# Performance work log

Hardware: AMD Instinct MI355X
Metric: run time of the kernel (lower is better)

## Reference

```python
import jax, jax.numpy as jnp
import numpy as np

DIM = 1024
DEPTH = 2
D_STATE = 16
EXPAND = 2            # standard Mamba expand factor -> d_inner = 2*dim
D_CONV = 4
DT_RANK = DIM // 16   # ceil(dim/16) = 64
D_INNER = DIM * EXPAND
BATCH = 2
SEQ = 1024


def setup_inputs() -> dict:
    key = jax.random.key(0)
    ks = jax.random.split(key, 8)
    def n(k, shape, scale):
        return jax.random.normal(k, shape, jnp.float32) * scale
    # A_log initialized as log(1..N) per channel (S4D-real init, as in mamba_ssm)
    A_log = jnp.tile(jnp.log(jnp.arange(1, D_STATE + 1, dtype=jnp.float32))[None, None, :],
                     (DEPTH, D_INNER, 1))
    return {
        "x": n(ks[0], (BATCH, SEQ, DIM), 1.0),
        "in_proj_w": n(ks[1], (DEPTH, 2 * D_INNER, DIM), DIM ** -0.5),
        "conv_w": n(ks[2], (DEPTH, D_INNER, D_CONV), D_CONV ** -0.5),
        "conv_b": jnp.zeros((DEPTH, D_INNER), jnp.float32),
        "x_proj_w": n(ks[3], (DEPTH, DT_RANK + 2 * D_STATE, D_INNER), D_INNER ** -0.5),
        "dt_proj_w": n(ks[4], (DEPTH, D_INNER, DT_RANK), DT_RANK ** -0.5),
        "dt_proj_b": n(ks[5], (DEPTH, D_INNER), 0.1),
        "A_log": A_log,
        "D": jnp.ones((DEPTH, D_INNER), jnp.float32),
        "out_proj_w": n(ks[6], (DEPTH, DIM, D_INNER), D_INNER ** -0.5),
    }


def _mamba_layer(x, in_w, cw, cb, xp_w, dtw, dtb, A_log, Dp, ow):
    # x: [B, L, dim]
    Bsz = x.shape[0]
    xz = jnp.einsum('bld,ed->ble', x, in_w)            # [B, L, 2*d_inner]
    xi, z = jnp.split(xz, 2, axis=-1)
    # causal depthwise conv1d over time
    xc = jnp.transpose(xi, (0, 2, 1))                  # [B, d_inner, L]
    xc = jax.lax.conv_general_dilated(xc, cw[:, None, :], (1,), [(D_CONV - 1, 0)],
                                      feature_group_count=D_INNER)
    xc = xc + cb[None, :, None]
    xc = jax.nn.silu(jnp.transpose(xc, (0, 2, 1)))     # [B, L, d_inner]
    # input-dependent dt, B, C
    x_dbl = jnp.einsum('bld,ed->ble', xc, xp_w)        # [B, L, dt_rank+2*N]
    dt_raw = x_dbl[..., :DT_RANK]
    Bm = x_dbl[..., DT_RANK:DT_RANK + D_STATE]         # [B, L, N]
    Cm = x_dbl[..., DT_RANK + D_STATE:]                # [B, L, N]
    dt = jax.nn.softplus(jnp.einsum('blr,dr->bld', dt_raw, dtw) + dtb)  # [B, L, d_inner]
    A = -jnp.exp(A_log)                                # [d_inner, N]
    dA = jnp.exp(dt[..., None] * A[None, None])        # [B, L, d_inner, N]
    dBu = dt[..., None] * Bm[:, :, None, :] * xc[..., None]

    def step(h, inp):
        dA_t, dBu_t, C_t = inp
        h = dA_t * h + dBu_t                           # [B, d_inner, N]
        y = jnp.einsum('bdn,bn->bd', h, C_t)
        return h, y

    h0 = jnp.zeros((Bsz, D_INNER, D_STATE), x.dtype)
    _, ys = jax.lax.scan(step, h0,
                         (dA.transpose(1, 0, 2, 3), dBu.transpose(1, 0, 2, 3),
                          Cm.transpose(1, 0, 2)))
    y = ys.transpose(1, 0, 2) + Dp[None, None, :] * xc
    y = y * jax.nn.silu(z)
    return jnp.einsum('bld,od->blo', y, ow)


def reference(x, in_proj_w, conv_w, conv_b, x_proj_w, dt_proj_w, dt_proj_b, A_log, D, out_proj_w):
    for i in range(DEPTH):
        x = _mamba_layer(x, in_proj_w[i], conv_w[i], conv_b[i], x_proj_w[i],
                         dt_proj_w[i], dt_proj_b[i], A_log[i], D[i], out_proj_w[i])
    return x
```

## Files before the change

kernel.cpp:

```cpp
#include <hip/hip_runtime.h>
#include <hip/hip_bf16.h>

typedef __hip_bfloat16 bf16;
typedef __attribute__((ext_vector_type(8))) short short8;
typedef __attribute__((ext_vector_type(4))) short shortx4;
typedef __attribute__((ext_vector_type(4))) float floatx4;

#define BATCH   2
#define SEQ     1024
#define DIM     1024
#define D_INNER 2048
#define D_STATE 16
#define DT_RANK 64
#define MROWS   (BATCH * SEQ)
#define CHUNK   32
#define NCHUNK  (SEQ / CHUNK)

__device__ __forceinline__ float bf2f(bf16 x) { return __bfloat162float(x); }
__device__ __forceinline__ bf16  f2bf(float x) { return __float2bfloat16(x); }
__device__ __forceinline__ short bfbits(float x) {
    bf16 b = __float2bfloat16(x); short s; __builtin_memcpy(&s, &b, 2); return s;
}
__device__ __forceinline__ float bits2f(short s) {
    bf16 b; __builtin_memcpy(&b, &s, 2); return __bfloat162float(b);
}

__device__ __forceinline__ void ld_lds16(const void* g, void* l) {
    __builtin_amdgcn_global_load_lds(
        (const __attribute__((address_space(1))) void*)g,
        (__attribute__((address_space(3))) void*)l, 16, 0, 0);
}

__device__ __forceinline__ void cast4(const float* in, short* o, int i) {
    floatx4 v = ((const floatx4*)in)[i];
    shortx4 r;
    r.x = bfbits(v.x); r.y = bfbits(v.y); r.z = bfbits(v.z); r.w = bfbits(v.w);
    ((shortx4*)o)[i] = r;
}
__global__ __launch_bounds__(256) void cast3_k(
    const float* __restrict__ a, short* __restrict__ oa, int na4,
    const float* __restrict__ b, short* __restrict__ ob, int nb4,
    const float* __restrict__ c, short* __restrict__ oc, int nc4)
{
    int i = blockIdx.x * 256 + threadIdx.x;
    if (i < na4) cast4(a, oa, i);
    else if (i - na4 < nb4) cast4(b, ob, i - na4);
    else if (i - na4 - nb4 < nc4) cast4(c, oc, i - na4 - nb4);
}

__device__ __forceinline__ short8 ld8_any(const void* p, size_t eoff, int is_f32) {
    if (is_f32) {
        const float* f = (const float*)p + eoff;
        floatx4 a = *(const floatx4*)f;
        floatx4 b = *(const floatx4*)(f + 4);
        short8 r;
        r[0] = bfbits(a[0]); r[1] = bfbits(a[1]); r[2] = bfbits(a[2]); r[3] = bfbits(a[3]);
        r[4] = bfbits(b[0]); r[5] = bfbits(b[1]); r[6] = bfbits(b[2]); r[7] = bfbits(b[3]);
        return r;
    } else {
        return *(const short8*)((const bf16*)p + eoff);
    }
}

__global__ __launch_bounds__(256) void gemm128(
    const bf16* __restrict__ A, int lda,
    const bf16* __restrict__ B, int ldb,
    float* __restrict__ Cf, bf16* __restrict__ Cb, int ldc,
    int kchunk, size_t psize)
{
    __shared__ short As[4][128 * 32];
    __shared__ short Bs[4][128 * 32];
    const int tid  = threadIdx.x;
    const int wave = tid >> 6;
    const int lane = tid & 63;
    const int m0 = blockIdx.y * 128;
    const int n0 = blockIdx.x * 128;
    const int wm = (wave & 1) * 64;
    const int wn = (wave >> 1) * 64;
    const int r16  = lane & 15;
    const int quad = lane >> 4;
    const int r0   = tid >> 2;
    const int csw   = (((tid & 3) ^ ((r0 >> 1) & 3)) << 3);
    const int swoff = ((quad ^ ((r16 >> 1) & 3)) << 3);
    const int kbeg = blockIdx.z * kchunk;
    const int nk   = kchunk >> 5;

    floatx4 acc[4][4] = {};

    auto STAGE = [&](int buf, int kk) {
        ld_lds16(A + (size_t)(m0 + r0) * lda + kk + csw,      &As[buf][tid * 8]);
        ld_lds16(A + (size_t)(m0 + r0 + 64) * lda + kk + csw, &As[buf][(tid + 256) * 8]);
        ld_lds16(B + (size_t)(n0 + r0) * ldb + kk + csw,      &Bs[buf][tid * 8]);
        ld_lds16(B + (size_t)(n0 + r0 + 64) * ldb + kk + csw, &Bs[buf][(tid + 256) * 8]);
    };
    auto COMPUTE = [&](int buf) {
        const short* Ab = As[buf];
        const short* Bb = Bs[buf];
        short8 af[4], bg[4];
#pragma unroll
        for (int i = 0; i < 4; i++) {
            af[i] = *(const short8*)(Ab + (wm + i * 16 + r16) * 32 + swoff);
            bg[i] = *(const short8*)(Bb + (wn + i * 16 + r16) * 32 + swoff);
        }
        __builtin_amdgcn_s_setprio(1);
#pragma unroll
        for (int i = 0; i < 4; i++)
#pragma unroll
            for (int j = 0; j < 4; j++)
                acc[i][j] = __builtin_amdgcn_mfma_f32_16x16x32_bf16(af[i], bg[j], acc[i][j], 0, 0, 0);
        __builtin_amdgcn_s_setprio(0);
    };

    STAGE(0, kbeg);
    STAGE(1, kbeg + 32);
    int it = 0;
    for (; it < nk - 2; ++it) {
        STAGE((it + 2) & 3, kbeg + (it + 2) * 32);
        asm volatile("s_waitcnt vmcnt(8) lgkmcnt(0)" ::: "memory");
        __builtin_amdgcn_s_barrier();
        __builtin_amdgcn_sched_barrier(0);
        COMPUTE(it & 3);
    }
    asm volatile("s_waitcnt vmcnt(4) lgkmcnt(0)" ::: "memory");
    __builtin_amdgcn_s_barrier();
    __builtin_amdgcn_sched_barrier(0);
    COMPUTE(it & 3);
    ++it;
    asm volatile("s_waitcnt vmcnt(0) lgkmcnt(0)" ::: "memory");
    __builtin_amdgcn_s_barrier();
    __builtin_amdgcn_sched_barrier(0);
    COMPUTE(it & 3);

    float* Cfp = Cf ? Cf + (size_t)blockIdx.z * psize : nullptr;
#pragma unroll
    for (int i = 0; i < 4; i++)
#pragma unroll
        for (int j = 0; j < 4; j++) {
            int gm = m0 + wm + i * 16 + quad * 4;
            int gn = n0 + wn + j * 16 + r16;
#pragma unroll
            for (int r = 0; r < 4; r++) {
                size_t o = (size_t)(gm + r) * ldc + gn;
                float v = acc[i][j][r];
                if (Cfp) Cfp[o] = v;
                if (Cb) Cb[o] = f2bf(v);
            }
        }
}

__global__ __launch_bounds__(256) void gemm_bt(
    const void* __restrict__ A, int a_f32, int lda,
    const void* __restrict__ B, int b_f32, int ldb,
    float* __restrict__ Cf, bf16* __restrict__ Cb, int ldc,
    int N, int K, size_t psize,
    const float* __restrict__ bias, int act)
{
    __shared__ short As[2][64][40];
    __shared__ short Bs[2][64][40];
    const int m0   = blockIdx.y * 64;
    const int n0   = blockIdx.x * 64;
    const int tid  = threadIdx.x;
    const int wave = tid >> 6;
    const int lane = tid & 63;
    const int srow = tid >> 2;
    const int scol = (tid & 3) << 3;
    const int r16  = lane & 15;
    const int quad = lane >> 4;
    const int kbeg = blockIdx.z * K;
    const int nst  = K >> 5;
    const int gn_b = n0 + srow;
    const bool bok = (gn_b < N);

    floatx4 acc[4] = {};

    short8 av = ld8_any(A, (size_t)(m0 + srow) * lda + kbeg + scol, a_f32);
    short8 bv = {};
    if (bok) bv = ld8_any(B, (size_t)gn_b * ldb + kbeg + scol, b_f32);

    for (int s = 0; s < nst; ++s) {
        const int cur = s & 1;
        *(short8*)(&As[cur][srow][scol]) = av;
        *(short8*)(&Bs[cur][srow][scol]) = bv;
        __syncthreads();
        if (s + 1 < nst) {
            int k1 = kbeg + (s + 1) * 32;
            av = ld8_any(A, (size_t)(m0 + srow) * lda + k1 + scol, a_f32);
            if (bok) bv = ld8_any(B, (size_t)gn_b * ldb + k1 + scol, b_f32);
        }
        short8 af = *(const short8*)(&As[cur][wave * 16 + r16][quad * 8]);
#pragma unroll
        for (int nt = 0; nt < 4; nt++) {
            short8 bq = *(const short8*)(&Bs[cur][nt * 16 + r16][quad * 8]);
            acc[nt] = __builtin_amdgcn_mfma_f32_16x16x32_bf16(af, bq, acc[nt], 0, 0, 0);
        }
    }

    float* Cfp = Cf ? Cf + (size_t)blockIdx.z * psize : nullptr;
#pragma unroll
    for (int nt = 0; nt < 4; nt++) {
        int gn = n0 + nt * 16 + r16;
        if (gn >= N) continue;
        float bsv = bias ? bias[gn] : 0.f;
#pragma unroll
        for (int r = 0; r < 4; r++) {
            int gm = m0 + wave * 16 + quad * 4 + r;
            float v = acc[nt][r] + bsv;
            if (act == 1) v = (v > 20.f) ? v : log1pf(__expf(v));
            size_t o = (size_t)gm * ldc + gn;
            if (Cfp) Cfp[o] = v;
            if (Cb) Cb[o] = f2bf(v);
        }
    }
}

__global__ __launch_bounds__(256) void reduceN_k(
    const float* __restrict__ part, size_t psize, int n, int np,
    float* __restrict__ of, bf16* __restrict__ ob)
{
    int i = blockIdx.x * 256 + threadIdx.x;
    if (i >= n) return;
    float v = 0.f;
    for (int j = 0; j < np; j++) v += part[i + (size_t)j * psize];
    if (of) of[i] = v;
    if (ob) ob[i] = f2bf(v);
}

__global__ __launch_bounds__(256) void conv_silu_k(
    const bf16* __restrict__ xz, const float* __restrict__ cw,
    const float* __restrict__ cb, bf16* __restrict__ xcb)
{
    int idx = blockIdx.x * 256 + threadIdx.x;
    int d   = (idx & 255) << 3;
    int bt  = idx >> 8;
    int t   = bt & (SEQ - 1);

    float s[8];
    floatx4 cb0 = *(const floatx4*)(cb + d);
    floatx4 cb1 = *(const floatx4*)(cb + d + 4);
#pragma unroll
    for (int i = 0; i < 4; i++) { s[i] = cb0[i]; s[i + 4] = cb1[i]; }

    floatx4 w[8];
#pragma unroll
    for (int i = 0; i < 8; i++) w[i] = *(const floatx4*)(cw + (d + i) * 4);

#pragma unroll
    for (int j = 0; j < 4; j++) {
        int tt = t - 3 + j;
        if (tt >= 0) {
            short8 v = *(const short8*)&xz[(size_t)(bt - 3 + j) * 4096 + d];
#pragma unroll
            for (int i = 0; i < 8; i++) s[i] += w[i][j] * bits2f(v[i]);
        }
    }
    short8 r;
#pragma unroll
    for (int i = 0; i < 8; i++) {
        float sig = 1.f / (1.f + __expf(-s[i]));
        r[i] = bfbits(s[i] * sig);
    }
    *(short8*)&xcb[(size_t)bt * D_INNER + d] = r;
}

__global__ __launch_bounds__(256) void scan1_k(
    const float* __restrict__ dtf, const bf16* __restrict__ xcb,
    const float* __restrict__ xdbl, const float* __restrict__ Alog,
    float* __restrict__ chunk_sdt, float* __restrict__ chunk_S)
{
    __shared__ float dt_s[CHUNK][256];
    __shared__ short xc_s[CHUNK][256];
    __shared__ float B_s[CHUNK][16];
    const int tid = threadIdx.x;
    const int d0  = blockIdx.x * 256;
    const int d   = d0 + tid;
    const int b   = blockIdx.y;
    const int c   = blockIdx.z;
    const size_t rbase = (size_t)b * SEQ + c * CHUNK;

#pragma unroll 4
    for (int t = 0; t < CHUNK; t++) {
        dt_s[t][tid] = dtf[(rbase + t) * D_INNER + d0 + tid];
        ((short*)xc_s)[t * 256 + tid] = *(const short*)&xcb[(rbase + t) * D_INNER + d0 + tid];
    }
    for (int e = tid; e < CHUNK * 16; e += 256) {
        int t = e >> 4, n = e & 15;
        B_s[t][n] = xdbl[(rbase + t) * 96 + 64 + n];
    }
    float A[16];
#pragma unroll
    for (int n = 0; n < 16; n++) A[n] = -__expf(Alog[(size_t)d * 16 + n]);
    float h[16] = {};
    float sdt = 0.f;
    __syncthreads();

    for (int t = 0; t < CHUNK; t++) {
        float dtv = dt_s[t][tid];
        float u = dtv * bits2f(xc_s[t][tid]);
        sdt += dtv;
        floatx4 B0 = *(const floatx4*)&B_s[t][0];
        floatx4 B1 = *(const floatx4*)&B_s[t][4];
        floatx4 B2 = *(const floatx4*)&B_s[t][8];
        floatx4 B3 = *(const floatx4*)&B_s[t][12];
#pragma unroll
        for (int n = 0; n < 4; n++) {
            h[n]      = __expf(dtv * A[n])      * h[n]      + u * B0[n];
            h[n + 4]  = __expf(dtv * A[n + 4])  * h[n + 4]  + u * B1[n];
            h[n + 8]  = __expf(dtv * A[n + 8])  * h[n + 8]  + u * B2[n];
            h[n + 12] = __expf(dtv * A[n + 12]) * h[n + 12] + u * B3[n];
        }
    }
    chunk_sdt[(b * NCHUNK + c) * D_INNER + d] = sdt;
#pragma unroll
    for (int n = 0; n < 16; n++)
        chunk_S[((size_t)(b * NCHUNK + c) * 16 + n) * D_INNER + d] = h[n];
}

__global__ __launch_bounds__(256) void scanpre_k(
    const float* __restrict__ Alog, const float* __restrict__ chunk_sdt,
    float* __restrict__ chunk_S)
{
    const int d = blockIdx.x * 256 + threadIdx.x;
    const int b = blockIdx.y;
    const int n = blockIdx.z;
    const float Av = -__expf(Alog[(size_t)d * 16 + n]);
    float h = 0.f;
    for (int j = 0; j < NCHUNK; j++) {
        size_t si = ((size_t)(b * NCHUNK + j) * 16 + n) * D_INNER + d;
        float S   = chunk_S[si];
        float sdt = chunk_sdt[(b * NCHUNK + j) * D_INNER + d];
        chunk_S[si] = h;
        h = __expf(sdt * Av) * h + S;
    }
}

__global__ __launch_bounds__(256) void scan2_k(
    const float* __restrict__ dtf, const bf16* __restrict__ xcb,
    const float* __restrict__ xdbl, const bf16* __restrict__ xz,
    const float* __restrict__ Alog, const float* __restrict__ Dp,
    const float* __restrict__ chunk_S, bf16* __restrict__ yb)
{
    __shared__ float dt_s[CHUNK][256];
    __shared__ short xc_s[CHUNK][256];
    __shared__ float B_s[CHUNK][16];
    __shared__ float C_s[CHUNK][16];
    const int tid = threadIdx.x;
    const int d0  = blockIdx.x * 256;
    const int d   = d0 + tid;
    const int b   = blockIdx.y;
    const int c   = blockIdx.z;
    const size_t rbase = (size_t)b * SEQ + c * CHUNK;

#pragma unroll 4
    for (int t = 0; t < CHUNK; t++) {
        dt_s[t][tid] = dtf[(rbase + t) * D_INNER + d0 + tid];
        ((short*)xc_s)[t * 256 + tid] = *(const short*)&xcb[(rbase + t) * D_INNER + d0 + tid];
    }
    for (int e = tid; e < CHUNK * 16; e += 256) {
        int t = e >> 4, n = e & 15;
        B_s[t][n] = xdbl[(rbase + t) * 96 + 64 + n];
        C_s[t][n] = xdbl[(rbase + t) * 96 + 80 + n];
    }
    float A[16];
#pragma unroll
    for (int n = 0; n < 16; n++) A[n] = -__expf(Alog[(size_t)d * 16 + n]);

    float h[16];
#pragma unroll
    for (int n = 0; n < 16; n++)
        h[n] = chunk_S[((size_t)(b * NCHUNK + c) * 16 + n) * D_INNER + d];

    const float Dv = Dp[d];
    __syncthreads();

    for (int t = 0; t < CHUNK; t++) {
        size_t row = rbase + t;
        float dtv = dt_s[t][tid];
        float xcv = bits2f(xc_s[t][tid]);
        float u = dtv * xcv;
        floatx4 B0 = *(const floatx4*)&B_s[t][0];
        floatx4 B1 = *(const floatx4*)&B_s[t][4];
        floatx4 B2 = *(const floatx4*)&B_s[t][8];
        floatx4 B3 = *(const floatx4*)&B_s[t][12];
        floatx4 C0 = *(const floatx4*)&C_s[t][0];
        floatx4 C1 = *(const floatx4*)&C_s[t][4];
        floatx4 C2 = *(const floatx4*)&C_s[t][8];
        floatx4 C3 = *(const floatx4*)&C_s[t][12];
        float y = 0.f;
#pragma unroll
        for (int n = 0; n < 4; n++) {
            h[n]      = __expf(dtv * A[n])      * h[n]      + u * B0[n];
            h[n + 4]  = __expf(dtv * A[n + 4])  * h[n + 4]  + u * B1[n];
            h[n + 8]  = __expf(dtv * A[n + 8])  * h[n + 8]  + u * B2[n];
            h[n + 12] = __expf(dtv * A[n + 12]) * h[n + 12] + u * B3[n];
            y += h[n] * C0[n] + h[n + 4] * C1[n] + h[n + 8] * C2[n] + h[n + 12] * C3[n];
        }
        float zv = bf2f(xz[row * 4096 + 2048 + d]);
        y = (y + Dv * xcv) * (zv / (1.f + __expf(-zv)));
        yb[row * D_INNER + d] = f2bf(y);
    }
}

extern "C" void kernel_launch(void* const* d_in, const int* in_sizes, int n_in,
                              void* d_out, int out_size, void* d_ws, size_t ws_size,
                              hipStream_t stream)
{
    const float* x    = (const float*)d_in[0];
    const float* inw  = (const float*)d_in[1];
    const float* cw   = (const float*)d_in[2];
    const float* cb   = (const float*)d_in[3];
    const float* xpw  = (const float*)d_in[4];
    const float* dtw  = (const float*)d_in[5];
    const float* dtb  = (const float*)d_in[6];
    const float* Alog = (const float*)d_in[7];
    const float* Dp   = (const float*)d_in[8];
    const float* ow   = (const float*)d_in[9];
    float* out = (float*)d_out;

    char* p = (char*)d_ws;
    bf16*  xzb   = (bf16*)p;  p += (size_t)MROWS * 4096 * 2;
    bf16*  xcb   = (bf16*)p;  p += (size_t)MROWS * D_INNER * 2;
    float* xdblf = (float*)p; p += (size_t)MROWS * 96 * 4;
    float* dtf   = (float*)p; p += (size_t)MROWS * D_INNER * 4;
    bf16*  ybf   = (bf16*)p;  p += (size_t)MROWS * D_INNER * 2;
    bf16*  xmid  = (bf16*)p;  p += (size_t)MROWS * DIM * 2;
    float* csdt  = (float*)p; p += (size_t)BATCH * NCHUNK * D_INNER * 4;
    float* cS    = (float*)p; p += (size_t)BATCH * NCHUNK * 16 * D_INNER * 4;
    bf16*  xb    = (bf16*)p;  p += (size_t)MROWS * DIM * 2;
    bf16*  inwb  = (bf16*)p;  p += (size_t)2 * 2 * D_INNER * DIM * 2;
    bf16*  owb   = (bf16*)p;  p += (size_t)2 * DIM * D_INNER * 2;
    float* xprt  = (float*)p; p += (size_t)8 * MROWS * 96 * 4;
    float* oprt  = (float*)p; p += (size_t)4 * MROWS * DIM * 4;

    const size_t xp_psize = (size_t)MROWS * 96;
    const size_t op_psize = (size_t)MROWS * DIM;

    {
        int na4 = MROWS * DIM / 4;
        int nb4 = 2 * 2 * D_INNER * DIM / 4;
        int nc4 = 2 * DIM * D_INNER / 4;
        cast3_k<<<(na4 + nb4 + nc4 + 255) / 256, 256, 0, stream>>>(
            x, (short*)xb, na4, inw, (short*)inwb, nb4, ow, (short*)owb, nc4);
    }

    for (int l = 0; l < 2; l++) {
        const float* xpw_l = xpw + (size_t)l * 96 * D_INNER;
        const float* dtw_l = dtw + (size_t)l * D_INNER * DT_RANK;
        const float* Al    = Alog + (size_t)l * D_INNER * D_STATE;
        bf16* inwb_l = inwb + (size_t)l * 2 * D_INNER * DIM;
        bf16* owb_l  = owb  + (size_t)l * DIM * D_INNER;

        gemm128<<<dim3(32, 16, 1), 256, 0, stream>>>(
            (l == 0) ? xb : xmid, DIM, inwb_l, DIM,
            nullptr, xzb, 4096, DIM, 0);

        conv_silu_k<<<(MROWS * D_INNER / 8) / 256, 256, 0, stream>>>(
            xzb, cw + (size_t)l * D_INNER * 4, cb + (size_t)l * D_INNER, xcb);

        gemm_bt<<<dim3(2, 32, 8), 256, 0, stream>>>(
            xcb, 0, D_INNER, xpw_l, 1, D_INNER,
            xprt, nullptr, 96, 96, 256, xp_psize, nullptr, 0);
        reduceN_k<<<(MROWS * 96 + 255) / 256, 256, 0, stream>>>(
            xprt, xp_psize, MROWS * 96, 8, xdblf, nullptr);

        gemm_bt<<<dim3(32, 32), 256, 0, stream>>>(
            xdblf, 1, 96, dtw_l, 1, DT_RANK,
            dtf, nullptr, D_INNER, D_INNER, DT_RANK, 0,
            dtb + (size_t)l * D_INNER, 1);

        scan1_k<<<dim3(D_INNER / 256, BATCH, NCHUNK), 256, 0, stream>>>(
            dtf, xcb, xdblf, Al, csdt, cS);
        scanpre_k<<<dim3(D_INNER / 256, BATCH, D_STATE), 256, 0, stream>>>(
            Al, csdt, cS);
        scan2_k<<<dim3(D_INNER / 256, BATCH, NCHUNK), 256, 0, stream>>>(
            dtf, xcb, xdblf, xzb, Al, Dp + (size_t)l * D_INNER, cS, ybf);

        gemm128<<<dim3(8, 16, 4), 256, 0, stream>>>(
            ybf, D_INNER, owb_l, D_INNER,
            oprt, nullptr, DIM, D_INNER / 4, op_psize);
        reduceN_k<<<(MROWS * DIM + 255) / 256, 256, 0, stream>>>(
            oprt, op_psize, MROWS * DIM, 4,
            (l == 1) ? out : nullptr, (l == 0) ? xmid : nullptr);
    }
}
```

Before: 403.2 us.

## Fold x_proj split-K reduction into consumers and use triple-buffered GEMM pipeline

```diff
diff --git a/kernel.cpp b/kernel.cpp
--- a/kernel.cpp
+++ b/kernel.cpp
@@ -62,14 +62,28 @@
     }
 }
 
-__global__ __launch_bounds__(256) void gemm128(
+__device__ __forceinline__ short8 ld8_sum8(const float* p, size_t eoff, size_t pstride) {
+    floatx4 a = {}, b = {};
+#pragma unroll
+    for (int j = 0; j < 8; j++) {
+        const float* f = p + (size_t)j * pstride + eoff;
+        a += *(const floatx4*)f;
+        b += *(const floatx4*)(f + 4);
+    }
+    short8 r;
+    r[0] = bfbits(a[0]); r[1] = bfbits(a[1]); r[2] = bfbits(a[2]); r[3] = bfbits(a[3]);
+    r[4] = bfbits(b[0]); r[5] = bfbits(b[1]); r[6] = bfbits(b[2]); r[7] = bfbits(b[3]);
+    return r;
+}
+
+__global__ __launch_bounds__(256, 3) void gemm128(
     const bf16* __restrict__ A, int lda,
     const bf16* __restrict__ B, int ldb,
     float* __restrict__ Cf, bf16* __restrict__ Cb, int ldc,
     int kchunk, size_t psize)
 {
-    __shared__ short As[4][128 * 32];
-    __shared__ short Bs[4][128 * 32];
+    __shared__ short As[3][128 * 32];
+    __shared__ short Bs[3][128 * 32];
     const int tid  = threadIdx.x;
     const int wave = tid >> 6;
     const int lane = tid & 63;
@@ -113,23 +127,20 @@
 
     STAGE(0, kbeg);
     STAGE(1, kbeg + 32);
-    int it = 0;
-    for (; it < nk - 2; ++it) {
-        STAGE((it + 2) & 3, kbeg + (it + 2) * 32);
-        asm volatile("s_waitcnt vmcnt(8) lgkmcnt(0)" ::: "memory");
+    int cbuf = 0, sbuf = 2;
+    for (int it = 0; it < nk - 1; ++it) {
+        asm volatile("s_waitcnt vmcnt(4) lgkmcnt(0)" ::: "memory");
         __builtin_amdgcn_s_barrier();
         __builtin_amdgcn_sched_barrier(0);
-        COMPUTE(it & 3);
-    }
-    asm volatile("s_waitcnt vmcnt(4) lgkmcnt(0)" ::: "memory");
-    __builtin_amdgcn_s_barrier();
-    __builtin_amdgcn_sched_barrier(0);
-    COMPUTE(it & 3);
-    ++it;
+        if (it + 2 < nk) STAGE(sbuf, kbeg + (it + 2) * 32);
+        COMPUTE(cbuf);
+        cbuf = (cbuf == 2) ? 0 : cbuf + 1;
+        sbuf = (sbuf == 2) ? 0 : sbuf + 1;
+    }
     asm volatile("s_waitcnt vmcnt(0) lgkmcnt(0)" ::: "memory");
     __builtin_amdgcn_s_barrier();
     __builtin_amdgcn_sched_barrier(0);
-    COMPUTE(it & 3);
+    COMPUTE(cbuf);
 
     float* Cfp = Cf ? Cf + (size_t)blockIdx.z * psize : nullptr;
 #pragma unroll
@@ -149,7 +160,7 @@
 }
 
 __global__ __launch_bounds__(256) void gemm_bt(
-    const void* __restrict__ A, int a_f32, int lda,
+    const void* __restrict__ A, int a_f32, int lda, size_t a_pstride,
     const void* __restrict__ B, int b_f32, int ldb,
     float* __restrict__ Cf, bf16* __restrict__ Cb, int ldc,
     int N, int K, size_t psize,
@@ -173,7 +184,13 @@
 
     floatx4 acc[4] = {};
 
-    short8 av = ld8_any(A, (size_t)(m0 + srow) * lda + kbeg + scol, a_f32);
+    auto lda8 = [&](int k0) -> short8 {
+        size_t eoff = (size_t)(m0 + srow) * lda + k0 + scol;
+        if (a_f32 == 2) return ld8_sum8((const float*)A, eoff, a_pstride);
+        return ld8_any(A, eoff, a_f32);
+    };
+
+    short8 av = lda8(kbeg);
     short8 bv = {};
     if (bok) bv = ld8_any(B, (size_t)gn_b * ldb + kbeg + scol, b_f32);
 
@@ -184,7 +201,7 @@
         __syncthreads();
         if (s + 1 < nst) {
             int k1 = kbeg + (s + 1) * 32;
-            av = ld8_any(A, (size_t)(m0 + srow) * lda + k1 + scol, a_f32);
+            av = lda8(k1);
             if (bok) bv = ld8_any(B, (size_t)gn_b * ldb + k1 + scol, b_f32);
         }
         short8 af = *(const short8*)(&As[cur][wave * 16 + r16][quad * 8]);
@@ -264,7 +281,7 @@
 
 __global__ __launch_bounds__(256) void scan1_k(
     const float* __restrict__ dtf, const bf16* __restrict__ xcb,
-    const float* __restrict__ xdbl, const float* __restrict__ Alog,
+    const float* __restrict__ xprt, size_t xp_ps, const float* __restrict__ Alog,
     float* __restrict__ chunk_sdt, float* __restrict__ chunk_S)
 {
     __shared__ float dt_s[CHUNK][256];
@@ -284,7 +301,11 @@
     }
     for (int e = tid; e < CHUNK * 16; e += 256) {
         int t = e >> 4, n = e & 15;
-        B_s[t][n] = xdbl[(rbase + t) * 96 + 64 + n];
+        float s = 0.f;
+#pragma unroll
+        for (int j = 0; j < 8; j++)
+            s += xprt[(size_t)j * xp_ps + (rbase + t) * 96 + 64 + n];
+        B_s[t][n] = s;
     }
     float A[16];
 #pragma unroll
@@ -324,6 +345,7 @@
     const int n = blockIdx.z;
     const float Av = -__expf(Alog[(size_t)d * 16 + n]);
     float h = 0.f;
+#pragma unroll 4
     for (int j = 0; j < NCHUNK; j++) {
         size_t si = ((size_t)(b * NCHUNK + j) * 16 + n) * D_INNER + d;
         float S   = chunk_S[si];
@@ -335,7 +357,7 @@
 
 __global__ __launch_bounds__(256) void scan2_k(
     const float* __restrict__ dtf, const bf16* __restrict__ xcb,
-    const float* __restrict__ xdbl, const bf16* __restrict__ xz,
+    const float* __restrict__ xprt, size_t xp_ps, const bf16* __restrict__ xz,
     const float* __restrict__ Alog, const float* __restrict__ Dp,
     const float* __restrict__ chunk_S, bf16* __restrict__ yb)
 {
@@ -357,8 +379,14 @@
     }
     for (int e = tid; e < CHUNK * 16; e += 256) {
         int t = e >> 4, n = e & 15;
-        B_s[t][n] = xdbl[(rbase + t) * 96 + 64 + n];
-        C_s[t][n] = xdbl[(rbase + t) * 96 + 80 + n];
+        float sB = 0.f, sC = 0.f;
+#pragma unroll
+        for (int j = 0; j < 8; j++) {
+            sB += xprt[(size_t)j * xp_ps + (rbase + t) * 96 + 64 + n];
+            sC += xprt[(size_t)j * xp_ps + (rbase + t) * 96 + 80 + n];
+        }
+        B_s[t][n] = sB;
+        C_s[t][n] = sC;
     }
     float A[16];
 #pragma unroll
@@ -419,7 +447,6 @@
     char* p = (char*)d_ws;
     bf16*  xzb   = (bf16*)p;  p += (size_t)MROWS * 4096 * 2;
     bf16*  xcb   = (bf16*)p;  p += (size_t)MROWS * D_INNER * 2;
-    float* xdblf = (float*)p; p += (size_t)MROWS * 96 * 4;
     float* dtf   = (float*)p; p += (size_t)MROWS * D_INNER * 4;
     bf16*  ybf   = (bf16*)p;  p += (size_t)MROWS * D_INNER * 2;
     bf16*  xmid  = (bf16*)p;  p += (size_t)MROWS * DIM * 2;
@@ -457,22 +484,20 @@
             xzb, cw + (size_t)l * D_INNER * 4, cb + (size_t)l * D_INNER, xcb);
 
         gemm_bt<<<dim3(2, 32, 8), 256, 0, stream>>>(
-            xcb, 0, D_INNER, xpw_l, 1, D_INNER,
+            xcb, 0, D_INNER, 0, xpw_l, 1, D_INNER,
             xprt, nullptr, 96, 96, 256, xp_psize, nullptr, 0);
-        reduceN_k<<<(MROWS * 96 + 255) / 256, 256, 0, stream>>>(
-            xprt, xp_psize, MROWS * 96, 8, xdblf, nullptr);
 
         gemm_bt<<<dim3(32, 32), 256, 0, stream>>>(
-            xdblf, 1, 96, dtw_l, 1, DT_RANK,
+            xprt, 2, 96, xp_psize, dtw_l, 1, DT_RANK,
             dtf, nullptr, D_INNER, D_INNER, DT_RANK, 0,
             dtb + (size_t)l * D_INNER, 1);
 
         scan1_k<<<dim3(D_INNER / 256, BATCH, NCHUNK), 256, 0, stream>>>(
-            dtf, xcb, xdblf, Al, csdt, cS);
+            dtf, xcb, xprt, xp_psize, Al, csdt, cS);
         scanpre_k<<<dim3(D_INNER / 256, BATCH, D_STATE), 256, 0, stream>>>(
             Al, csdt, cS);
         scan2_k<<<dim3(D_INNER / 256, BATCH, NCHUNK), 256, 0, stream>>>(
-            dtf, xcb, xdblf, xzb, Al, Dp + (size_t)l * D_INNER, cS, ybf);
+            dtf, xcb, xprt, xp_psize, xzb, Al, Dp + (size_t)l * D_INNER, cS, ybf);
 
         gemm128<<<dim3(8, 16, 4), 256, 0, stream>>>(
             ybf, D_INNER, owb_l, D_INNER,
```

After: 419.9 us. +4.1%, slower.
